# Kernel tuning notes

Hardware: AMD Instinct MI355X
Metric: run time of the kernel (lower is better)

The kernel has to match this reference:

```python
import jax, jax.numpy as jnp
import numpy as np


def setup_inputs() -> dict:
    key = jax.random.key(0)
    ks = jax.random.split(key, 4)
    B, T, D, U = 64, 2048, 128, 128
    enc = jax.random.normal(ks[0], (B, T, D), dtype=jnp.float32)
    # Keras Dense default: glorot_uniform kernel, zero bias; use scaled normals here.
    W1_w = jax.random.normal(ks[1], (D, U), dtype=jnp.float32) / np.sqrt(D)
    W2_w = jax.random.normal(ks[2], (D, U), dtype=jnp.float32) / np.sqrt(D)
    V_w = jax.random.normal(ks[3], (U, 1), dtype=jnp.float32) / np.sqrt(U)
    return {
        "encoder_outputs": enc,
        "W1_w": W1_w,
        "W1_b": jnp.zeros((U,), jnp.float32),
        "W2_w": W2_w,
        "W2_b": jnp.zeros((U,), jnp.float32),
        "V_w": V_w,
        "V_b": jnp.zeros((1,), jnp.float32),
    }


def reference(encoder_outputs, W1_w, W1_b, W2_w, W2_b, V_w, V_b):
    # score = V(tanh(W1(x) + W2(x)))  -> [B, T, 1]
    # W1(x)+W2(x) == x @ (W1_w + W2_w) + (W1_b + W2_b); keep faithful but fused.
    h = jnp.tanh(jnp.einsum("btd,du->btu", encoder_outputs, W1_w) + W1_b
                 + jnp.einsum("btd,du->btu", encoder_outputs, W2_w) + W2_b)
    score = jnp.einsum("btu,uo->bto", h, V_w) + V_b  # [B, T, 1]
    attn = jax.nn.softmax(score, axis=1)             # softmax over sequence axis
    # context = sum_t attn[b,t,0] * x[b,t,:]
    context = jnp.einsum("bto,btd->bd", attn, encoder_outputs)
    return context
```

## Files before the change

### kernel.cpp

```cpp
#include <hip/hip_runtime.h>
#include <hip/hip_bf16.h>

#define DD 128
#define UU 128
#define SEQ_T 2048
#define ROWS 128
#define PART_STRIDE 132

typedef __attribute__((ext_vector_type(8))) short short8;
typedef __attribute__((ext_vector_type(4))) float f32x4;

__device__ __forceinline__ unsigned short f2bf(float f) {
  unsigned u = __float_as_uint(f);
  u += 0x7fffu + ((u >> 16) & 1u);
  return (unsigned short)(u >> 16);
}
__device__ __forceinline__ float bf2f(unsigned short s) {
  return __uint_as_float(((unsigned)s) << 16);
}
__device__ __forceinline__ float fast_tanh(float v) {
  float z = __expf(2.0f * v);
  return 1.0f - __fdividef(2.0f, z + 1.0f);
}

__global__ void prep_kernel(const float* __restrict__ W1w, const float* __restrict__ W1b,
                            const float* __restrict__ W2w, const float* __restrict__ W2b,
                            unsigned short* __restrict__ wt_g, float* __restrict__ bias_g)
{
  int i = blockIdx.x * 256 + threadIdx.x;
  int u = i >> 7, d = i & 127;
  float s = W1w[(size_t)d * UU + u] + W2w[(size_t)d * UU + u];
  wt_g[(size_t)u * DD + d] = f2bf(s);
  if (i < UU) bias_g[i] = W1b[i] + W2b[i];
}

__global__ __launch_bounds__(256, 3)
void fused_score_ctx(const float* __restrict__ x,
                     const unsigned short* __restrict__ wt_g,
                     const float* __restrict__ bias_g,
                     const float* __restrict__ Vw,
                     float* __restrict__ part)
{
  __shared__ __align__(16) unsigned short xs[ROWS * DD];
  __shared__ __align__(16) float spart[4][ROWS];
  __shared__ float slds[ROWS];
  __shared__ float pctx_red[4][DD];
  __shared__ float red[8];

  const int tid = threadIdx.x;
  const int blk = blockIdx.x;
  const int rowbase = blk * ROWS;
  const int w = tid >> 6, l = tid & 63, lx = l & 15, lq = l >> 4;

  short8 Bf[2][4];
  float vs[2], bs[2];
  #pragma unroll
  for (int nf = 0; nf < 2; ++nf) {
    const int u = 32 * w + 16 * nf + lx;
    vs[nf] = Vw[u];
    bs[nf] = bias_g[u];
    #pragma unroll
    for (int kf = 0; kf < 4; ++kf)
      Bf[nf][kf] = *reinterpret_cast<const short8*>(
          wt_g + (size_t)u * DD + 32 * kf + 8 * lq);
  }

  #pragma unroll
  for (int it = 0; it < 8; ++it) {
    int F = tid + 256 * it;
    int row = F >> 4, g = F & 15;
    const float* src = x + (size_t)(rowbase + row) * DD + g * 8;
    const float4 v0 = *reinterpret_cast<const float4*>(src);
    const float4 v1 = *reinterpret_cast<const float4*>(src + 4);
    short8 pk;
    pk[0] = (short)f2bf(v0.x); pk[1] = (short)f2bf(v0.y);
    pk[2] = (short)f2bf(v0.z); pk[3] = (short)f2bf(v0.w);
    pk[4] = (short)f2bf(v1.x); pk[5] = (short)f2bf(v1.y);
    pk[6] = (short)f2bf(v1.z); pk[7] = (short)f2bf(v1.w);
    *reinterpret_cast<short8*>(xs + row * DD + ((g ^ (row & 15)) << 3)) = pk;
  }
  __syncthreads();

  f32x4 acc[8][2];
  #pragma unroll
  for (int mf = 0; mf < 8; ++mf) {
    acc[mf][0] = (f32x4){0.f, 0.f, 0.f, 0.f};
    acc[mf][1] = (f32x4){0.f, 0.f, 0.f, 0.f};
  }
  #pragma unroll
  for (int kf = 0; kf < 4; ++kf) {
    const int gs8 = ((4 * kf + lq) ^ lx) << 3;
    #pragma unroll
    for (int mf = 0; mf < 8; ++mf) {
      short8 a = *reinterpret_cast<const short8*>(xs + (16 * mf + lx) * DD + gs8);
      acc[mf][0] = __builtin_amdgcn_mfma_f32_16x16x32_bf16(a, Bf[0][kf], acc[mf][0], 0, 0, 0);
      acc[mf][1] = __builtin_amdgcn_mfma_f32_16x16x32_bf16(a, Bf[1][kf], acc[mf][1], 0, 0, 0);
    }
  }

  #pragma unroll
  for (int mf = 0; mf < 8; ++mf) {
    f32x4 pv;
    #pragma unroll
    for (int r = 0; r < 4; ++r) {
      float p = vs[0] * fast_tanh(acc[mf][0][r] + bs[0])
              + vs[1] * fast_tanh(acc[mf][1][r] + bs[1]);
      p += __shfl_xor(p, 1);
      p += __shfl_xor(p, 2);
      p += __shfl_xor(p, 4);
      p += __shfl_xor(p, 8);
      pv[r] = p;
    }
    if (lx == 0)
      *reinterpret_cast<f32x4*>(&spart[w][16 * mf + 4 * lq]) = pv;
  }
  __syncthreads();

  const int rr = tid & 127;
  float sv = (spart[0][rr] + spart[1][rr]) + (spart[2][rr] + spart[3][rr]);
  float m = sv;
  #pragma unroll
  for (int off = 1; off < 64; off <<= 1) m = fmaxf(m, __shfl_xor(m, off));
  if (l == 0) red[w] = m;
  __syncthreads();
  m = fmaxf(fmaxf(red[0], red[1]), fmaxf(red[2], red[3]));

  float e = (tid < 128) ? __expf(sv - m) : 0.0f;
  float lsum = e;
  #pragma unroll
  for (int off = 1; off < 64; off <<= 1) lsum += __shfl_xor(lsum, off);
  if (l == 0) red[4 + w] = lsum;
  __syncthreads();
  lsum = (red[4] + red[5]) + (red[6] + red[7]);

  if (tid < 128) slds[tid] = e;
  __syncthreads();

  {
    const int gd = tid & 15;
    const int tg = tid >> 4;
    float ca[8];
    #pragma unroll
    for (int e2 = 0; e2 < 8; ++e2) ca[e2] = 0.0f;
    #pragma unroll
    for (int k = 0; k < 8; ++k) {
      int t = tg * 8 + k;
      float wgt = slds[t];
      short8 xv = *reinterpret_cast<const short8*>(xs + t * DD + ((gd ^ (t & 15)) << 3));
      #pragma unroll
      for (int e2 = 0; e2 < 8; ++e2)
        ca[e2] = fmaf(wgt, bf2f((unsigned short)xv[e2]), ca[e2]);
    }
    #pragma unroll
    for (int e2 = 0; e2 < 8; ++e2) {
      ca[e2] += __shfl_xor(ca[e2], 16);
      ca[e2] += __shfl_xor(ca[e2], 32);
    }
    if ((l >> 4) == 0) {
      #pragma unroll
      for (int e2 = 0; e2 < 8; ++e2) pctx_red[w][gd * 8 + e2] = ca[e2];
    }
  }
  __syncthreads();

  float* prec = part + (size_t)blk * PART_STRIDE;
  if (tid < 128) {
    float c0 = (pctx_red[0][tid] + pctx_red[1][tid]) +
               (pctx_red[2][tid] + pctx_red[3][tid]);
    prec[4 + tid] = c0;
  }
  if (tid == 0) { prec[0] = m; prec[1] = lsum; }
}

__global__ void combine_kernel(const float* __restrict__ part,
                               float* __restrict__ out, int chunks)
{
  int b = blockIdx.x;
  int d = threadIdx.x;
  float mg = -3.0e38f;
  for (int i = 0; i < chunks; ++i)
    mg = fmaxf(mg, part[(size_t)(b * chunks + i) * PART_STRIDE]);
  float den = 0.0f, num = 0.0f;
  for (int i = 0; i < chunks; ++i) {
    const float* p = part + (size_t)(b * chunks + i) * PART_STRIDE;
    float sc = __expf(p[0] - mg);
    den = fmaf(sc, p[1], den);
    num = fmaf(sc, p[4 + d], num);
  }
  out[(size_t)b * DD + d] = __fdividef(num, den);
}

extern "C" void kernel_launch(void* const* d_in, const int* in_sizes, int n_in,
                              void* d_out, int out_size, void* d_ws, size_t ws_size,
                              hipStream_t stream)
{
  const float* x   = (const float*)d_in[0];
  const float* W1w = (const float*)d_in[1];
  const float* W1b = (const float*)d_in[2];
  const float* W2w = (const float*)d_in[3];
  const float* W2b = (const float*)d_in[4];
  const float* Vw  = (const float*)d_in[5];

  const int bt = in_sizes[0] / DD;
  const int nblk = bt / ROWS;
  const int B = bt / SEQ_T;
  const int chunks = SEQ_T / ROWS;

  float* part = (float*)d_ws;
  unsigned short* wt_g = (unsigned short*)((char*)d_ws + 540672);
  float* bias_g = (float*)((char*)d_ws + 540672 + 32768);

  prep_kernel<<<64, 256, 0, stream>>>(W1w, W1b, W2w, W2b, wt_g, bias_g);
  fused_score_ctx<<<nblk, 256, 0, stream>>>(x, wt_g, bias_g, Vw, part);
  combine_kernel<<<B, 128, 0, stream>>>(part, (float*)d_out, chunks);
}
```

Baseline: 40.60 us.

## Halve rows per block, prefetch x into registers, simplify softmax reduction

Shrinks each block's tile from 128 to 64 sequence rows, which doubles the grid, halves LDS use, and raises the occupancy hint to 4 blocks per CU. The global loads of x are issued before the weight fragment loads so their latency overlaps. With 64 rows a single wavefront holds every score, so the cross-wave max/sum reduction and its two barriers are removed. The cost is twice as many partial records for the combine kernel to process, plus extra register pressure from the prefetched x values.

```diff
diff --git a/kernel.cpp b/kernel.cpp
--- a/kernel.cpp
+++ b/kernel.cpp
@@ -4,7 +4,7 @@
 #define DD 128
 #define UU 128
 #define SEQ_T 2048
-#define ROWS 128
+#define ROWS 64
 #define PART_STRIDE 132
 
 typedef __attribute__((ext_vector_type(8))) short short8;
@@ -34,7 +34,7 @@
   if (i < UU) bias_g[i] = W1b[i] + W2b[i];
 }
 
-__global__ __launch_bounds__(256, 3)
+__global__ __launch_bounds__(256, 4)
 void fused_score_ctx(const float* __restrict__ x,
                      const unsigned short* __restrict__ wt_g,
                      const float* __restrict__ bias_g,
@@ -44,14 +44,23 @@
   __shared__ __align__(16) unsigned short xs[ROWS * DD];
   __shared__ __align__(16) float spart[4][ROWS];
   __shared__ float slds[ROWS];
-  __shared__ float pctx_red[4][DD];
-  __shared__ float red[8];
+  __shared__ __align__(16) float pctx_red[4][DD];
 
   const int tid = threadIdx.x;
   const int blk = blockIdx.x;
   const int rowbase = blk * ROWS;
   const int w = tid >> 6, l = tid & 63, lx = l & 15, lq = l >> 4;
 
+  float4 xr[8];
+  #pragma unroll
+  for (int it = 0; it < 4; ++it) {
+    int F = tid + 256 * it;
+    int row = F >> 4, g = F & 15;
+    const float* src = x + (size_t)(rowbase + row) * DD + g * 8;
+    xr[2 * it]     = *reinterpret_cast<const float4*>(src);
+    xr[2 * it + 1] = *reinterpret_cast<const float4*>(src + 4);
+  }
+
   short8 Bf[2][4];
   float vs[2], bs[2];
   #pragma unroll
@@ -66,12 +75,10 @@
   }
 
   #pragma unroll
-  for (int it = 0; it < 8; ++it) {
+  for (int it = 0; it < 4; ++it) {
     int F = tid + 256 * it;
     int row = F >> 4, g = F & 15;
-    const float* src = x + (size_t)(rowbase + row) * DD + g * 8;
-    const float4 v0 = *reinterpret_cast<const float4*>(src);
-    const float4 v1 = *reinterpret_cast<const float4*>(src + 4);
+    float4 v0 = xr[2 * it], v1 = xr[2 * it + 1];
     short8 pk;
     pk[0] = (short)f2bf(v0.x); pk[1] = (short)f2bf(v0.y);
     pk[2] = (short)f2bf(v0.z); pk[3] = (short)f2bf(v0.w);
@@ -81,9 +88,9 @@
   }
   __syncthreads();
 
-  f32x4 acc[8][2];
-  #pragma unroll
-  for (int mf = 0; mf < 8; ++mf) {
+  f32x4 acc[4][2];
+  #pragma unroll
+  for (int mf = 0; mf < 4; ++mf) {
     acc[mf][0] = (f32x4){0.f, 0.f, 0.f, 0.f};
     acc[mf][1] = (f32x4){0.f, 0.f, 0.f, 0.f};
   }
@@ -91,7 +98,7 @@
   for (int kf = 0; kf < 4; ++kf) {
     const int gs8 = ((4 * kf + lq) ^ lx) << 3;
     #pragma unroll
-    for (int mf = 0; mf < 8; ++mf) {
+    for (int mf = 0; mf < 4; ++mf) {
       short8 a = *reinterpret_cast<const short8*>(xs + (16 * mf + lx) * DD + gs8);
       acc[mf][0] = __builtin_amdgcn_mfma_f32_16x16x32_bf16(a, Bf[0][kf], acc[mf][0], 0, 0, 0);
       acc[mf][1] = __builtin_amdgcn_mfma_f32_16x16x32_bf16(a, Bf[1][kf], acc[mf][1], 0, 0, 0);
@@ -99,8 +106,7 @@
   }
 
   #pragma unroll
-  for (int mf = 0; mf < 8; ++mf) {
-    f32x4 pv;
+  for (int mf = 0; mf < 4; ++mf) {
     #pragma unroll
     for (int r = 0; r < 4; ++r) {
       float p = vs[0] * fast_tanh(acc[mf][0][r] + bs[0])
@@ -109,31 +115,20 @@
       p += __shfl_xor(p, 2);
       p += __shfl_xor(p, 4);
       p += __shfl_xor(p, 8);
-      pv[r] = p;
-    }
-    if (lx == 0)
-      *reinterpret_cast<f32x4*>(&spart[w][16 * mf + 4 * lq]) = pv;
-  }
-  __syncthreads();
-
-  const int rr = tid & 127;
-  float sv = (spart[0][rr] + spart[1][rr]) + (spart[2][rr] + spart[3][rr]);
+      if (lx == 0) spart[w][16 * mf + 4 * lq + r] = p;
+    }
+  }
+  __syncthreads();
+
+  float sv = (spart[0][l] + spart[1][l]) + (spart[2][l] + spart[3][l]);
   float m = sv;
   #pragma unroll
   for (int off = 1; off < 64; off <<= 1) m = fmaxf(m, __shfl_xor(m, off));
-  if (l == 0) red[w] = m;
-  __syncthreads();
-  m = fmaxf(fmaxf(red[0], red[1]), fmaxf(red[2], red[3]));
-
-  float e = (tid < 128) ? __expf(sv - m) : 0.0f;
+  float e = __expf(sv - m);
   float lsum = e;
   #pragma unroll
   for (int off = 1; off < 64; off <<= 1) lsum += __shfl_xor(lsum, off);
-  if (l == 0) red[4 + w] = lsum;
-  __syncthreads();
-  lsum = (red[4] + red[5]) + (red[6] + red[7]);
-
-  if (tid < 128) slds[tid] = e;
+  if (w == 0) slds[l] = e;
   __syncthreads();
 
   {
@@ -143,8 +138,8 @@
     #pragma unroll
     for (int e2 = 0; e2 < 8; ++e2) ca[e2] = 0.0f;
     #pragma unroll
-    for (int k = 0; k < 8; ++k) {
-      int t = tg * 8 + k;
+    for (int k = 0; k < 4; ++k) {
+      int t = tg * 4 + k;
       float wgt = slds[t];
       short8 xv = *reinterpret_cast<const short8*>(xs + t * DD + ((gd ^ (t & 15)) << 3));
       #pragma unroll
@@ -206,9 +201,10 @@
   const int B = bt / SEQ_T;
   const int chunks = SEQ_T / ROWS;
 
+  const size_t part_bytes = (size_t)nblk * PART_STRIDE * sizeof(float);
   float* part = (float*)d_ws;
-  unsigned short* wt_g = (unsigned short*)((char*)d_ws + 540672);
-  float* bias_g = (float*)((char*)d_ws + 540672 + 32768);
+  unsigned short* wt_g = (unsigned short*)((char*)d_ws + part_bytes);
+  float* bias_g = (float*)((char*)d_ws + part_bytes + 32768);
 
   prep_kernel<<<64, 256, 0, stream>>>(W1w, W1b, W2w, W2b, wt_g, bias_g);
   fused_score_ctx<<<nblk, 256, 0, stream>>>(x, wt_g, bias_g, Vw, part);
```

New measurement: 44.16 us. +8.8%, slower.
